# Optimization experiments

Hardware: AMD Instinct MI355X
Metric: run time of the kernel (lower is better)

Reference implementation:

```python
import jax, jax.numpy as jnp
import numpy as np

N_NODES = 100000
N_EDGES = 1600000
N_GRAPHS = 2048
HID = 64
IN_F = 14
N_CLS = 2
EPS = 1e-5


def _gcn_conv(x, row, col, w_edge, W, b, n_nodes):
    # PyG GCNConv with add_self_loops=True, normalize=True.
    xw = x @ W  # [N, out]
    # degree on target nodes, self-loop contributes weight 1
    deg = jnp.zeros((n_nodes,), x.dtype).at[col].add(w_edge) + 1.0
    dinv = deg ** -0.5
    norm = dinv[row] * w_edge * dinv[col]  # [E]
    out = jnp.zeros_like(xw).at[col].add(norm[:, None] * xw[row])
    out = out + (dinv * dinv)[:, None] * xw  # self-loop term
    return out + b


def _bn_relu(x, gamma, beta):
    mean = jnp.mean(x, axis=0)
    var = jnp.var(x, axis=0)  # biased, as PyTorch BN training normalization
    y = gamma * (x - mean) * jax.lax.rsqrt(var + EPS) + beta
    return jax.nn.relu(y)


def setup_inputs() -> dict:
    key = jax.random.key(0)
    ks = jax.random.split(key, 8)
    x = jax.random.normal(ks[0], (N_NODES, IN_F), dtype=jnp.float32)
    edge_index = jax.random.randint(ks[1], (2, N_EDGES), 0, N_NODES, dtype=jnp.int64)
    batch = jnp.sort(jax.random.randint(ks[2], (N_NODES,), 0, N_GRAPHS, dtype=jnp.int64))
    edge_weight = jnp.ones((N_EDGES,), dtype=jnp.float32)
    def lin(k, fi, fo):
        s = 1.0 / np.sqrt(fi)
        kw, kb = jax.random.split(k)
        return (jax.random.uniform(kw, (fi, fo), jnp.float32, -s, s),
                jax.random.uniform(kb, (fo,), jnp.float32, -s, s))
    W1, b1 = lin(ks[3], IN_F, HID)
    W2, b2 = lin(ks[4], HID, HID)
    W3, b3 = lin(ks[5], HID, HID)
    fcW, fcb = lin(ks[6], HID, N_CLS)
    g = jnp.ones((HID,), jnp.float32)
    z = jnp.zeros((HID,), jnp.float32)
    return {
        "x": x, "edge_index": edge_index, "batch": batch, "edge_weight": edge_weight,
        "W1": W1, "b1": b1, "W2": W2, "b2": b2, "W3": W3, "b3": b3,
        "g1": g, "bt1": z, "g2": g, "bt2": z, "g3": g, "bt3": z,
        "fcW": fcW, "fcb": fcb,
    }


def reference(x, edge_index, batch, edge_weight, W1, b1, W2, b2, W3, b3,
              g1, bt1, g2, bt2, g3, bt3, fcW, fcb):
    row, col = edge_index[0], edge_index[1]
    n = x.shape[0]
    h = _bn_relu(_gcn_conv(x, row, col, edge_weight, W1, b1, n), g1, bt1)
    h = _bn_relu(_gcn_conv(h, row, col, edge_weight, W2, b2, n), g2, bt2)
    h = _bn_relu(_gcn_conv(h, row, col, edge_weight, W3, b3, n), g3, bt3)
    node_embs = h  # dropout p=0 is identity
    graph_emb = jax.ops.segment_sum(node_embs, batch, num_segments=N_GRAPHS)
    out = graph_emb @ fcW + fcb
    return (out, node_embs, graph_emb)
```

## Files before the change

kernel.cpp:

```cpp
#include <hip/hip_runtime.h>
#include <hip/hip_fp16.h>

#define N_NODES 100000
#define N_EDGES 1600000
#define EMAX2   1700000
#define N_GRAPHS 2048
#define HID 64
#define IN_F 14
#define N_CLS 2
#define EPS 1e-5f

#define BSHIFT 9
#define NBUCK 196
#define ABLOCKS 256
#define CHUNK (N_EDGES / ABLOCKS)

#define NBLK2 128
#define NCHUNK2 ((N_NODES + NBLK2 - 1) / NBLK2)

typedef _Float16 half_t;
typedef _Float16 half8 __attribute__((ext_vector_type(8)));
typedef float f32x4 __attribute__((ext_vector_type(4)));

#define GSTRIDE ((size_t)N_NODES * 16)


__global__ __launch_bounds__(256) void histA_kernel(const int* __restrict__ col,
                                                    int* __restrict__ histG) {
    __shared__ int hl[NBUCK];
    for (int i = threadIdx.x; i < NBUCK; i += 256) hl[i] = 0;
    __syncthreads();
    int e0 = blockIdx.x * CHUNK;
    for (int e = e0 + threadIdx.x; e < e0 + CHUNK; e += 256)
        atomicAdd(&hl[col[e] >> BSHIFT], 1);
    __syncthreads();
    for (int i = threadIdx.x; i < NBUCK; i += 256)
        histG[i * ABLOCKS + blockIdx.x] = hl[i];
}

__global__ __launch_bounds__(256) void scanS1_kernel(const int* __restrict__ histG,
                                                     int* __restrict__ bsumA) {
    __shared__ int ls[256];
    ls[threadIdx.x] = histG[blockIdx.x * 256 + threadIdx.x];
    __syncthreads();
    for (int off = 128; off > 0; off >>= 1) {
        if (threadIdx.x < off) ls[threadIdx.x] += ls[threadIdx.x + off];
        __syncthreads();
    }
    if (threadIdx.x == 0) bsumA[blockIdx.x] = ls[0];
}

__global__ __launch_bounds__(512) void topscan_kernel(int* __restrict__ bsum, int nb) {
    __shared__ int ls[512];
    int t = threadIdx.x;
    int v = (t < nb) ? bsum[t] : 0;
    ls[t] = v;
    __syncthreads();
    for (int off = 1; off < 512; off <<= 1) {
        int x = ls[t];
        if (t >= off) x += ls[t - off];
        __syncthreads();
        ls[t] = x;
        __syncthreads();
    }
    if (t < nb) bsum[t] = ls[t] - v;
}

__global__ __launch_bounds__(256) void scanS3_kernel(int* __restrict__ histG,
                                                     const int* __restrict__ bsumA,
                                                     int* __restrict__ ptr) {
    __shared__ int ls[256];
    int idx = blockIdx.x * 256 + threadIdx.x;
    int v = histG[idx];
    ls[threadIdx.x] = v;
    __syncthreads();
    for (int off = 1; off < 256; off <<= 1) {
        int x = ls[threadIdx.x];
        if (threadIdx.x >= off) x += ls[threadIdx.x - off];
        __syncthreads();
        ls[threadIdx.x] = x;
        __syncthreads();
    }
    histG[idx] = ls[threadIdx.x] - v + bsumA[blockIdx.x];
    if (blockIdx.x == 0 && threadIdx.x == 0) ptr[N_NODES] = N_EDGES;
}

__global__ __launch_bounds__(256) void scatterA_kernel(const int* __restrict__ row,
                                                       const int* __restrict__ col,
                                                       const float* __restrict__ w,
                                                       const int* __restrict__ histG,
                                                       int2* __restrict__ EA) {
    __shared__ int cur[NBUCK];
    for (int i = threadIdx.x; i < NBUCK; i += 256)
        cur[i] = histG[i * ABLOCKS + blockIdx.x];
    __syncthreads();
    int e0 = blockIdx.x * CHUNK;
    for (int e = e0 + threadIdx.x; e < e0 + CHUNK; e += 256) {
        int c = col[e];
        int r = row[e];
        int fx = (int)__float2uint_rn(w[e] * 8192.0f);
        int pos = atomicAdd(&cur[c >> BSHIFT], 1);
        EA[pos] = make_int2(r, (fx << 17) | c);
    }
}

__global__ __launch_bounds__(256) void bucketA_kernel(const int2* __restrict__ EA,
                                                      const int* __restrict__ bsumA,
                                                      int* __restrict__ ptr,
                                                      float* __restrict__ dinv) {
    __shared__ int hist[512], wsum[512];
    int b = blockIdx.x;
    int beg = bsumA[b];
    int end = (b == NBUCK - 1) ? N_EDGES : bsumA[b + 1];
    int i0 = threadIdx.x, i1 = threadIdx.x + 256;
    hist[i0] = 0; hist[i1] = 0;
    wsum[i0] = 0; wsum[i1] = 0;
    __syncthreads();
    for (int e = beg + threadIdx.x; e < end; e += 256) {
        int2 ed = EA[e];
        int c9 = ed.y & 511;
        atomicAdd(&hist[c9], 1);
        atomicAdd(&wsum[c9], (int)((unsigned int)ed.y >> 17));
    }
    __syncthreads();
    int cnt0 = hist[i0], cnt1 = hist[i1];
    for (int off = 1; off < 512; off <<= 1) {
        int v0 = hist[i0], v1 = hist[i1];
        int a0 = (i0 >= off) ? hist[i0 - off] : 0;
        int a1 = (i1 >= off) ? hist[i1 - off] : 0;
        __syncthreads();
        hist[i0] = v0 + a0;
        hist[i1] = v1 + a1;
        __syncthreads();
    }
    int excl0 = hist[i0] - cnt0, excl1 = hist[i1] - cnt1;
    int col0 = (b << BSHIFT) + i0, col1 = (b << BSHIFT) + i1;
    if (col0 < N_NODES) {
        ptr[col0] = beg + excl0;
        dinv[col0] = rsqrtf(1.0f + (float)wsum[i0] * (1.0f / 8192.0f));
    }
    if (col1 < N_NODES) {
        ptr[col1] = beg + excl1;
        dinv[col1] = rsqrtf(1.0f + (float)wsum[i1] * (1.0f / 8192.0f));
    }
}


__global__ __launch_bounds__(256) void histD_kernel(const int* __restrict__ ptr,
                                                    int* __restrict__ histD) {
    __shared__ int hl[2048];
    for (int i = threadIdx.x; i < 2048; i += 256) hl[i] = 0;
    __syncthreads();
    int n0 = blockIdx.x * NCHUNK2;
    int n1 = n0 + NCHUNK2; if (n1 > N_NODES) n1 = N_NODES;
    for (int n = n0 + threadIdx.x; n < n1; n += 256) {
        int d = ptr[n + 1] - ptr[n];
        if (d > 255) d = 255;
        atomicAdd(&hl[((threadIdx.x & 7) << 8) + d], 1);
    }
    __syncthreads();
    int s = 0;
#pragma unroll
    for (int c = 0; c < 8; c++) s += hl[(c << 8) + threadIdx.x];
    histD[threadIdx.x * NBLK2 + blockIdx.x] = s;
}

__global__ __launch_bounds__(128) void scanD1_kernel(const int* __restrict__ histD,
                                                     int* __restrict__ rowTot) {
    __shared__ int ls[128];
    ls[threadIdx.x] = histD[blockIdx.x * NBLK2 + threadIdx.x];
    __syncthreads();
    for (int off = 64; off > 0; off >>= 1) {
        if (threadIdx.x < off) ls[threadIdx.x] += ls[threadIdx.x + off];
        __syncthreads();
    }
    if (threadIdx.x == 0) rowTot[blockIdx.x] = ls[0];
}

__global__ __launch_bounds__(256) void topscanD_kernel(const int* __restrict__ rowTot,
                                                       int* __restrict__ nodeExcl,
                                                       int* __restrict__ edgeExcl,
                                                       int* __restrict__ ptrS) {
    __shared__ int a[256], b[256];
    int t = threadIdx.x;
    int cnt = rowTot[t];
    int dpad = (t + 1) & ~1;
    int ec = cnt * dpad;
    a[t] = cnt; b[t] = ec;
    __syncthreads();
    for (int off = 1; off < 256; off <<= 1) {
        int va = a[t], vb = b[t];
        if (t >= off) { va += a[t - off]; vb += b[t - off]; }
        __syncthreads();
        a[t] = va; b[t] = vb;
        __syncthreads();
    }
    nodeExcl[t] = a[t] - cnt;
    edgeExcl[t] = b[t] - ec;
    if (t == 255) ptrS[N_NODES] = b[255];
}

__global__ __launch_bounds__(128) void scanD3_kernel(int* __restrict__ histD,
                                                     const int* __restrict__ nodeExcl) {
    __shared__ int ls[128];
    int idx = blockIdx.x * NBLK2 + threadIdx.x;
    int v = histD[idx];
    ls[threadIdx.x] = v;
    __syncthreads();
    for (int off = 1; off < 128; off <<= 1) {
        int x = ls[threadIdx.x];
        if (threadIdx.x >= off) x += ls[threadIdx.x - off];
        __syncthreads();
        ls[threadIdx.x] = x;
        __syncthreads();
    }
    histD[idx] = ls[threadIdx.x] - v + nodeExcl[blockIdx.x];
}

__global__ __launch_bounds__(256) void scatterD_kernel(const int* __restrict__ ptr,
                                                       const int* __restrict__ histD,
                                                       const int* __restrict__ nodeExcl,
                                                       const int* __restrict__ edgeExcl,
                                                       int* __restrict__ perm,
                                                       int* __restrict__ ptrS,
                                                       int* __restrict__ newbase) {
    __shared__ int cur[256];
    cur[threadIdx.x] = histD[threadIdx.x * NBLK2 + blockIdx.x];
    __syncthreads();
    int n0 = blockIdx.x * NCHUNK2;
    int n1 = n0 + NCHUNK2; if (n1 > N_NODES) n1 = N_NODES;
    for (int n = n0 + threadIdx.x; n < n1; n += 256) {
        int d = ptr[n + 1] - ptr[n];
        if (d > 255) d = 255;
        int dpad = (d + 1) & ~1;
        int pos = atomicAdd(&cur[d], 1);
        int ebase = edgeExcl[d] + (pos - nodeExcl[d]) * dpad;
        perm[pos] = n;
        ptrS[pos] = ebase;
        newbase[n] = ebase;
    }
}

__global__ __launch_bounds__(256) void bucketB_kernel(const int2* __restrict__ EA,
                                                      const int* __restrict__ bsumA,
                                                      const int* __restrict__ newbase,
                                                      const float* __restrict__ dinv,
                                                      unsigned int* __restrict__ srcoff,
                                                      half_t* __restrict__ normh) {
    __shared__ int cur[512];
    int b = blockIdx.x;
    int beg = bsumA[b];
    int end = (b == NBUCK - 1) ? N_EDGES : bsumA[b + 1];
    int i0 = threadIdx.x, i1 = threadIdx.x + 256;
    int col0 = (b << BSHIFT) + i0, col1 = (b << BSHIFT) + i1;
    cur[i0] = (col0 < N_NODES) ? newbase[col0] : 0;
    cur[i1] = (col1 < N_NODES) ? newbase[col1] : 0;
    __syncthreads();
    for (int e = beg + threadIdx.x; e < end; e += 256) {
        int2 ed = EA[e];
        int c = ed.y & 0x1ffff;
        float w = (float)((unsigned int)ed.y >> 17) * (1.0f / 8192.0f);
        float nrm = dinv[ed.x] * w * dinv[c];
        int pos = atomicAdd(&cur[c & 511], 1);
        srcoff[pos] = (unsigned int)ed.x << 5;
        normh[pos] = (half_t)nrm;
    }
}


template <int K>
__global__ __launch_bounds__(256) void gemm_kernel(const float* __restrict__ h,
                                                   const float* __restrict__ W,
                                                   half_t* __restrict__ xw, int n_nodes) {
    int f = threadIdx.x & 63;
    float wcol[K];
#pragma unroll
    for (int k = 0; k < K; k++) wcol[k] = W[k * HID + f];
    half_t* xg = xw + (size_t)(f >> 4) * GSTRIDE + (f & 15);
    int wave = (blockIdx.x * blockDim.x + threadIdx.x) >> 6;
    int nwaves = (gridDim.x * blockDim.x) >> 6;
    for (int n = wave; n < n_nodes; n += nwaves) {
        const float* hr = h + (size_t)n * K;
        float acc = 0.f;
#pragma unroll
        for (int k = 0; k < K; k++) acc += hr[k] * wcol[k];
        xg[(size_t)n * 16] = (half_t)acc;
    }
}

__global__ __launch_bounds__(256) void gemm_bn_mfma_kernel(const half_t* __restrict__ h,
                                                           const float* __restrict__ W,
                                                           const float* __restrict__ stats,
                                                           const float* __restrict__ gamma,
                                                           const float* __restrict__ beta,
                                                           half_t* __restrict__ xw, int n_nodes) {
    __shared__ float sc_s[HID], sh_s[HID];
    if (threadIdx.x < 64) {
        float mean = stats[threadIdx.x] * (1.0f / N_NODES);
        float var = stats[64 + threadIdx.x] * (1.0f / N_NODES) - mean * mean;
        float sc = gamma[threadIdx.x] * rsqrtf(var + EPS);
        sc_s[threadIdx.x] = sc;
        sh_s[threadIdx.x] = beta[threadIdx.x] - mean * sc;
    }
    __syncthreads();
    int lane = threadIdx.x & 63;
    int col16 = lane & 15;
    int quad = lane >> 4;

    float scA[2][8], shA[2][8];
#pragma unroll
    for (int kh = 0; kh < 2; kh++)
#pragma unroll
        for (int j = 0; j < 8; j++) {
            int k = kh * 32 + quad * 8 + j;
            scA[kh][j] = sc_s[k];
            shA[kh][j] = sh_s[k];
        }

    half8 bfrag[4][2];
#pragma unroll
    for (int t = 0; t < 4; t++)
#pragma unroll
        for (int kh = 0; kh < 2; kh++)
#pragma unroll
            for (int j = 0; j < 8; j++) {
                int k = kh * 32 + quad * 8 + j;
                bfrag[t][kh][j] = (half_t)W[k * HID + t * 16 + col16];
            }

    int wave = (blockIdx.x * blockDim.x + threadIdx.x) >> 6;
    int nwaves = (gridDim.x * blockDim.x) >> 6;
    int ntiles = n_nodes >> 4;
    for (int tIdx = wave; tIdx < ntiles; tIdx += nwaves) {
        int n0 = tIdx << 4;
        half8 afrag[2];
#pragma unroll
        for (int kh = 0; kh < 2; kh++) {
            int k0 = kh * 32 + quad * 8;
            const half_t* hp = h + (size_t)(k0 >> 4) * GSTRIDE
                                 + (size_t)(n0 + col16) * 16 + (k0 & 15);
            half8 raw = *(const half8*)hp;
#pragma unroll
            for (int j = 0; j < 8; j++) {
                float v = (float)raw[j] * scA[kh][j] + shA[kh][j];
                afrag[kh][j] = (half_t)fmaxf(v, 0.f);
            }
        }
        f32x4 acc[4];
#pragma unroll
        for (int t = 0; t < 4; t++) {
            f32x4 z = {0.f, 0.f, 0.f, 0.f};
            acc[t] = __builtin_amdgcn_mfma_f32_16x16x32_f16(afrag[0], bfrag[t][0], z, 0, 0, 0);
            acc[t] = __builtin_amdgcn_mfma_f32_16x16x32_f16(afrag[1], bfrag[t][1], acc[t], 0, 0, 0);
        }
#pragma unroll
        for (int t = 0; t < 4; t++) {
            half_t* xg = xw + (size_t)t * GSTRIDE;
#pragma unroll
            for (int r = 0; r < 4; r++) {
                int rowi = n0 + quad * 4 + r;
                xg[(size_t)rowi * 16 + col16] = (half_t)acc[t][r];
            }
        }
    }
}

template <bool LAST>
__global__ __launch_bounds__(256) void gather_stats_kernel(const int* __restrict__ ptrS,
                                                           const int* __restrict__ perm,
                                                           const unsigned int* __restrict__ srcoff,
                                                           const unsigned int* __restrict__ normu,
                                                           const half_t* __restrict__ xw,
                                                           const float* __restrict__ dinv,
                                                           const float* __restrict__ b,
                                                           half_t* __restrict__ hp,
                                                           float* __restrict__ hf,
                                                           float* __restrict__ stats,
                                                           int n_nodes) {
    int g = (blockIdx.x & 7) >> 1;
    int grank = ((blockIdx.x >> 3) << 1) | (blockIdx.x & 1);
    int lane16 = threadIdx.x & 15;
    int quadLocal = threadIdx.x >> 4;
    int quadId = grank * 16 + quadLocal;
    int nquads = (gridDim.x >> 2) * 16;

    const half_t* xg = xw + (size_t)g * GSTRIDE;
    const char* xgc = (const char*)xg;
    unsigned int loff = (unsigned int)(lane16 * 2);
    half_t* hpg = hp + (size_t)g * GSTRIDE;
    int f = g * 16 + lane16;
    float bf = b[f];
    int base = ((threadIdx.x & 63) >> 4) * 16;

    float s = 0.f, s2 = 0.f;
    for (int i = quadId; i < n_nodes; i += nquads) {
        int node = perm[i];
        int beg = ptrS[i];
        int c = ptrS[i + 1] - beg;
        __half2 acc0 = __float2half2_rn(0.f);
        __half2 acc1 = __float2half2_rn(0.f);
        for (int j0 = 0; j0 < c; j0 += 16) {
            int m = c - j0;
            if (m > 16) m = 16;
            int pairs = m >> 1;
            int ev = 0, nv = 0;
            if (lane16 < m) ev = (int)srcoff[beg + j0 + lane16];
            if (lane16 < pairs) nv = (int)normu[((beg + j0) >> 1) + lane16];
            int p = 0;
            for (; p + 2 <= pairs; p += 2) {
                unsigned int u0 = (unsigned int)__shfl(ev, base + 2 * p);
                unsigned int u1 = (unsigned int)__shfl(ev, base + 2 * p + 1);
                unsigned int u2 = (unsigned int)__shfl(ev, base + 2 * p + 2);
                unsigned int u3 = (unsigned int)__shfl(ev, base + 2 * p + 3);
                unsigned int nd0 = (unsigned int)__shfl(nv, base + p);
                unsigned int nd1 = (unsigned int)__shfl(nv, base + p + 1);
                __half h0 = *(const __half*)(xgc + (u0 + loff));
                __half h1 = *(const __half*)(xgc + (u1 + loff));
                __half h2 = *(const __half*)(xgc + (u2 + loff));
                __half h3 = *(const __half*)(xgc + (u3 + loff));
                __half2 n01 = *(__half2*)&nd0;
                __half2 n23 = *(__half2*)&nd1;
                acc0 = __hfma2(n01, __halves2half2(h0, h1), acc0);
                acc1 = __hfma2(n23, __halves2half2(h2, h3), acc1);
            }
            if (p < pairs) {
                unsigned int u0 = (unsigned int)__shfl(ev, base + 2 * p);
                unsigned int u1 = (unsigned int)__shfl(ev, base + 2 * p + 1);
                unsigned int nd0 = (unsigned int)__shfl(nv, base + p);
                __half h0 = *(const __half*)(xgc + (u0 + loff));
                __half h1 = *(const __half*)(xgc + (u1 + loff));
                __half2 n01 = *(__half2*)&nd0;
                acc0 = __hfma2(n01, __halves2half2(h0, h1), acc0);
            }
        }
        float accf = (__low2float(acc0) + __high2float(acc0))
                   + (__low2float(acc1) + __high2float(acc1));
        float di = dinv[node];
        float v = accf + di * di * (float)xg[(size_t)node * 16 + lane16] + bf;
        if (LAST)
            hf[(size_t)node * HID + f] = v;
        else
            hpg[(size_t)node * 16 + lane16] = (half_t)v;
        s += v;
        s2 += v * v;
    }
    __shared__ float ls[256], ls2[256];
    ls[threadIdx.x] = s;
    ls2[threadIdx.x] = s2;
    __syncthreads();
    if (threadIdx.x < 16) {
        float a = 0.f, aa = 0.f;
#pragma unroll
        for (int k = 0; k < 16; k++) {
            a += ls[k * 16 + threadIdx.x];
            aa += ls2[k * 16 + threadIdx.x];
        }
        atomicAdd(&stats[g * 16 + threadIdx.x], a);
        atomicAdd(&stats[64 + g * 16 + threadIdx.x], aa);
    }
}

__global__ __launch_bounds__(256) void bn_relu_seg_kernel(float* __restrict__ h,
                                                          const float* __restrict__ stats,
                                                          const float* __restrict__ gamma,
                                                          const float* __restrict__ beta,
                                                          const int* __restrict__ batch,
                                                          float* __restrict__ gemb,
                                                          int n_nodes) {
    int g = blockIdx.x * blockDim.x + threadIdx.x;
    int f = g & 63;
    int wave = g >> 6;
    int nwaves = (gridDim.x * blockDim.x) >> 6;
    int chunk = (n_nodes + nwaves - 1) / nwaves;
    int n0 = wave * chunk;
    int n1 = n0 + chunk;
    if (n1 > n_nodes) n1 = n_nodes;
    if (n0 >= n_nodes) return;
    float mean = stats[f] * (1.0f / N_NODES);
    float var = stats[64 + f] * (1.0f / N_NODES) - mean * mean;
    float sc = gamma[f] * rsqrtf(var + EPS);
    float sh = beta[f] - mean * sc;
    int curg = batch[n0];
    float racc = 0.f;
    for (int n = n0; n < n1; n++) {
        int bg = batch[n];
        if (bg != curg) {
            atomicAdd(&gemb[(size_t)curg * HID + f], racc);
            racc = 0.f;
            curg = bg;
        }
        size_t idx = (size_t)n * HID + f;
        float v = h[idx] * sc + sh;
        v = fmaxf(v, 0.f);
        h[idx] = v;
        racc += v;
    }
    atomicAdd(&gemb[(size_t)curg * HID + f], racc);
}

__global__ __launch_bounds__(256) void final_kernel(const float* __restrict__ gemb,
                                                    const float* __restrict__ fcW,
                                                    const float* __restrict__ fcb,
                                                    float* __restrict__ out) {
    int g = blockIdx.x * blockDim.x + threadIdx.x;
    if (g >= N_GRAPHS * N_CLS) return;
    int gr = g >> 1, c = g & 1;
    float acc = fcb[c];
#pragma unroll
    for (int k = 0; k < HID; k++) acc += gemb[gr * HID + k] * fcW[k * N_CLS + c];
    out[g] = acc;
}


extern "C" void kernel_launch(void* const* d_in, const int* in_sizes, int n_in,
                              void* d_out, int out_size, void* d_ws, size_t ws_size,
                              hipStream_t stream) {
    const float* x    = (const float*)d_in[0];
    const int*   ei   = (const int*)d_in[1];
    const int*   batch= (const int*)d_in[2];
    const float* ew   = (const float*)d_in[3];
    const float* W1   = (const float*)d_in[4];
    const float* b1   = (const float*)d_in[5];
    const float* W2   = (const float*)d_in[6];
    const float* b2   = (const float*)d_in[7];
    const float* W3   = (const float*)d_in[8];
    const float* b3   = (const float*)d_in[9];
    const float* g1   = (const float*)d_in[10];
    const float* bt1  = (const float*)d_in[11];
    const float* g2   = (const float*)d_in[12];
    const float* bt2  = (const float*)d_in[13];
    const float* g3   = (const float*)d_in[14];
    const float* bt3  = (const float*)d_in[15];
    const float* fcW  = (const float*)d_in[16];
    const float* fcb  = (const float*)d_in[17];

    const int* row = ei;
    const int* col = ei + N_EDGES;

    float* out_head  = (float*)d_out;
    float* node_embs = out_head + N_GRAPHS * N_CLS;
    float* gemb      = node_embs + (size_t)N_NODES * HID;

    char* bse = (char*)d_ws;
    half_t* xwh = (half_t*)bse;
    char* r1 = bse + (size_t)N_NODES * HID * 2;
    int2*   EA  = (int2*)r1;
    half_t* hpl = (half_t*)r1;
    char* r2 = r1 + (size_t)N_NODES * HID * 2;
    unsigned int* srcoff = (unsigned int*)r2;
    half_t* normh = (half_t*)(srcoff + EMAX2);
    char* r3 = r2 + (size_t)EMAX2 * 6;
    float* dinv  = (float*)r3;
    float* stats = dinv + N_NODES;
    int*   ptr   = (int*)(stats + 128);
    int*   histG = ptr + N_NODES + 1;
    int*   bsumA = histG + NBUCK * ABLOCKS;
    int*   histD = bsumA + NBUCK + 4;
    int*   rowTot = histD + 256 * NBLK2;
    int*   nodeExcl = rowTot + 256;
    int*   edgeExcl = nodeExcl + 256;
    int*   perm   = edgeExcl + 256;
    int*   newbase= perm + N_NODES;
    int*   ptrS   = newbase + N_NODES;

    const int B   = 256;
    const int gGS = 1024;
    const int gGA = 2048;

    histA_kernel<<<ABLOCKS, B, 0, stream>>>(col, histG);
    scanS1_kernel<<<NBUCK, B, 0, stream>>>(histG, bsumA);
    topscan_kernel<<<1, 512, 0, stream>>>(bsumA, NBUCK);
    scanS3_kernel<<<NBUCK, B, 0, stream>>>(histG, bsumA, ptr);
    scatterA_kernel<<<ABLOCKS, B, 0, stream>>>(row, col, ew, histG, EA);
    bucketA_kernel<<<NBUCK, B, 0, stream>>>(EA, bsumA, ptr, dinv);

    histD_kernel<<<NBLK2, B, 0, stream>>>(ptr, histD);
    scanD1_kernel<<<256, 128, 0, stream>>>(histD, rowTot);
    topscanD_kernel<<<1, 256, 0, stream>>>(rowTot, nodeExcl, edgeExcl, ptrS);
    scanD3_kernel<<<256, 128, 0, stream>>>(histD, nodeExcl);
    scatterD_kernel<<<NBLK2, B, 0, stream>>>(ptr, histD, nodeExcl, edgeExcl,
                                             perm, ptrS, newbase);
    hipMemsetAsync(srcoff, 0, (size_t)EMAX2 * 6, stream);
    bucketB_kernel<<<NBUCK, B, 0, stream>>>(EA, bsumA, newbase, dinv, srcoff, normh);

    float* h3 = node_embs;

    gemm_kernel<IN_F><<<gGS, B, 0, stream>>>(x, W1, xwh, N_NODES);
    hipMemsetAsync(stats, 0, 128 * sizeof(float), stream);
    gather_stats_kernel<false><<<gGA, B, 0, stream>>>(ptrS, perm, srcoff,
                                                      (const unsigned int*)normh, xwh,
                                                      dinv, b1, hpl, h3, stats, N_NODES);

    gemm_bn_mfma_kernel<<<gGS, B, 0, stream>>>(hpl, W2, stats, g1, bt1, xwh, N_NODES);
    hipMemsetAsync(stats, 0, 128 * sizeof(float), stream);
    gather_stats_kernel<false><<<gGA, B, 0, stream>>>(ptrS, perm, srcoff,
                                                      (const unsigned int*)normh, xwh,
                                                      dinv, b2, hpl, h3, stats, N_NODES);

    gemm_bn_mfma_kernel<<<gGS, B, 0, stream>>>(hpl, W3, stats, g2, bt2, xwh, N_NODES);
    hipMemsetAsync(stats, 0, 128 * sizeof(float), stream);
    gather_stats_kernel<true><<<gGA, B, 0, stream>>>(ptrS, perm, srcoff,
                                                     (const unsigned int*)normh, xwh,
                                                     dinv, b3, hpl, h3, stats, N_NODES);

    hipMemsetAsync(gemb, 0, (size_t)N_GRAPHS * HID * sizeof(float), stream);
    bn_relu_seg_kernel<<<gGS, B, 0, stream>>>(h3, stats, g3, bt3, batch, gemb, N_NODES);

    final_kernel<<<(N_GRAPHS * N_CLS + B - 1) / B, B, 0, stream>>>(gemb, fcW, fcb, out_head);
}
```

Before: 415.0 us.

## Pad per-node edge lists to multiples of four and use vector loads in gather

Edge slots per node are now padded to a multiple of four instead of two. This lets the gather loop read source offsets and norms with 128-bit and 64-bit per-lane vector loads instead of cooperative loads plus shuffles, and the loop is unrolled over 16 edges with four accumulators. The per-layer stats memsets are merged into a single upfront memset of three separate stats buffers, and the gemb memset is moved up with them. The cost is more padded zero edges (larger buffer, wasted loads) and redundant per-lane index loads across the 16 lanes.

```diff
diff --git a/kernel.cpp b/kernel.cpp
--- a/kernel.cpp
+++ b/kernel.cpp
@@ -3,7 +3,7 @@
 
 #define N_NODES 100000
 #define N_EDGES 1600000
-#define EMAX2   1700000
+#define EMAX4   1900000
 #define N_GRAPHS 2048
 #define HID 64
 #define IN_F 14
@@ -21,8 +21,17 @@
 typedef _Float16 half_t;
 typedef _Float16 half8 __attribute__((ext_vector_type(8)));
 typedef float f32x4 __attribute__((ext_vector_type(4)));
+typedef unsigned int u32;
+typedef u32 u32x4 __attribute__((ext_vector_type(4)));
+typedef u32 u32x2 __attribute__((ext_vector_type(2)));
 
 #define GSTRIDE ((size_t)N_NODES * 16)
+
+__device__ __forceinline__ __half2 u32_as_half2(u32 u) {
+    union { u32 u; __half2 h; } c;
+    c.u = u;
+    return c.h;
+}
 
 
 __global__ __launch_bounds__(256) void histA_kernel(const int* __restrict__ col,
@@ -184,7 +193,7 @@
     __shared__ int a[256], b[256];
     int t = threadIdx.x;
     int cnt = rowTot[t];
-    int dpad = (t + 1) & ~1;
+    int dpad = (t + 3) & ~3;
     int ec = cnt * dpad;
     a[t] = cnt; b[t] = ec;
     __syncthreads();
@@ -232,7 +241,7 @@
     for (int n = n0 + threadIdx.x; n < n1; n += 256) {
         int d = ptr[n + 1] - ptr[n];
         if (d > 255) d = 255;
-        int dpad = (d + 1) & ~1;
+        int dpad = (d + 3) & ~3;
         int pos = atomicAdd(&cur[d], 1);
         int ebase = edgeExcl[d] + (pos - nodeExcl[d]) * dpad;
         perm[pos] = n;
@@ -369,7 +378,7 @@
 __global__ __launch_bounds__(256) void gather_stats_kernel(const int* __restrict__ ptrS,
                                                            const int* __restrict__ perm,
                                                            const unsigned int* __restrict__ srcoff,
-                                                           const unsigned int* __restrict__ normu,
+                                                           const half_t* __restrict__ normh,
                                                            const half_t* __restrict__ xw,
                                                            const float* __restrict__ dinv,
                                                            const float* __restrict__ b,
@@ -387,54 +396,65 @@
     const half_t* xg = xw + (size_t)g * GSTRIDE;
     const char* xgc = (const char*)xg;
     unsigned int loff = (unsigned int)(lane16 * 2);
+    const unsigned int* np = (const unsigned int*)normh;
     half_t* hpg = hp + (size_t)g * GSTRIDE;
     int f = g * 16 + lane16;
     float bf = b[f];
-    int base = ((threadIdx.x & 63) >> 4) * 16;
 
     float s = 0.f, s2 = 0.f;
     for (int i = quadId; i < n_nodes; i += nquads) {
         int node = perm[i];
-        int beg = ptrS[i];
-        int c = ptrS[i + 1] - beg;
-        __half2 acc0 = __float2half2_rn(0.f);
-        __half2 acc1 = __float2half2_rn(0.f);
-        for (int j0 = 0; j0 < c; j0 += 16) {
-            int m = c - j0;
-            if (m > 16) m = 16;
-            int pairs = m >> 1;
-            int ev = 0, nv = 0;
-            if (lane16 < m) ev = (int)srcoff[beg + j0 + lane16];
-            if (lane16 < pairs) nv = (int)normu[((beg + j0) >> 1) + lane16];
-            int p = 0;
-            for (; p + 2 <= pairs; p += 2) {
-                unsigned int u0 = (unsigned int)__shfl(ev, base + 2 * p);
-                unsigned int u1 = (unsigned int)__shfl(ev, base + 2 * p + 1);
-                unsigned int u2 = (unsigned int)__shfl(ev, base + 2 * p + 2);
-                unsigned int u3 = (unsigned int)__shfl(ev, base + 2 * p + 3);
-                unsigned int nd0 = (unsigned int)__shfl(nv, base + p);
-                unsigned int nd1 = (unsigned int)__shfl(nv, base + p + 1);
-                __half h0 = *(const __half*)(xgc + (u0 + loff));
-                __half h1 = *(const __half*)(xgc + (u1 + loff));
-                __half h2 = *(const __half*)(xgc + (u2 + loff));
-                __half h3 = *(const __half*)(xgc + (u3 + loff));
-                __half2 n01 = *(__half2*)&nd0;
-                __half2 n23 = *(__half2*)&nd1;
-                acc0 = __hfma2(n01, __halves2half2(h0, h1), acc0);
-                acc1 = __hfma2(n23, __halves2half2(h2, h3), acc1);
-            }
-            if (p < pairs) {
-                unsigned int u0 = (unsigned int)__shfl(ev, base + 2 * p);
-                unsigned int u1 = (unsigned int)__shfl(ev, base + 2 * p + 1);
-                unsigned int nd0 = (unsigned int)__shfl(nv, base + p);
-                __half h0 = *(const __half*)(xgc + (u0 + loff));
-                __half h1 = *(const __half*)(xgc + (u1 + loff));
-                __half2 n01 = *(__half2*)&nd0;
-                acc0 = __hfma2(n01, __halves2half2(h0, h1), acc0);
-            }
-        }
-        float accf = (__low2float(acc0) + __high2float(acc0))
-                   + (__low2float(acc1) + __high2float(acc1));
+        int j = ptrS[i];
+        int cend = ptrS[i + 1];
+        __half2 z2 = __float2half2_rn(0.f);
+        __half2 acc0 = z2, acc1 = z2, acc2 = z2, acc3 = z2;
+        for (; j + 16 <= cend; j += 16) {
+            u32x4 s0 = *(const u32x4*)(srcoff + j);
+            u32x4 s1 = *(const u32x4*)(srcoff + j + 4);
+            u32x4 s2v = *(const u32x4*)(srcoff + j + 8);
+            u32x4 s3 = *(const u32x4*)(srcoff + j + 12);
+            int jh = j >> 1;
+            u32x2 n0 = *(const u32x2*)(np + jh);
+            u32x2 n1 = *(const u32x2*)(np + jh + 2);
+            u32x2 n2 = *(const u32x2*)(np + jh + 4);
+            u32x2 n3 = *(const u32x2*)(np + jh + 6);
+            __half h0 = *(const __half*)(xgc + (s0.x + loff));
+            __half h1 = *(const __half*)(xgc + (s0.y + loff));
+            __half h2 = *(const __half*)(xgc + (s0.z + loff));
+            __half h3 = *(const __half*)(xgc + (s0.w + loff));
+            __half h4 = *(const __half*)(xgc + (s1.x + loff));
+            __half h5 = *(const __half*)(xgc + (s1.y + loff));
+            __half h6 = *(const __half*)(xgc + (s1.z + loff));
+            __half h7 = *(const __half*)(xgc + (s1.w + loff));
+            __half h8 = *(const __half*)(xgc + (s2v.x + loff));
+            __half h9 = *(const __half*)(xgc + (s2v.y + loff));
+            __half hA = *(const __half*)(xgc + (s2v.z + loff));
+            __half hB = *(const __half*)(xgc + (s2v.w + loff));
+            __half hC = *(const __half*)(xgc + (s3.x + loff));
+            __half hD = *(const __half*)(xgc + (s3.y + loff));
+            __half hE = *(const __half*)(xgc + (s3.z + loff));
+            __half hF = *(const __half*)(xgc + (s3.w + loff));
+            acc0 = __hfma2(u32_as_half2(n0.x), __halves2half2(h0, h1), acc0);
+            acc0 = __hfma2(u32_as_half2(n0.y), __halves2half2(h2, h3), acc0);
+            acc1 = __hfma2(u32_as_half2(n1.x), __halves2half2(h4, h5), acc1);
+            acc1 = __hfma2(u32_as_half2(n1.y), __halves2half2(h6, h7), acc1);
+            acc2 = __hfma2(u32_as_half2(n2.x), __halves2half2(h8, h9), acc2);
+            acc2 = __hfma2(u32_as_half2(n2.y), __halves2half2(hA, hB), acc2);
+            acc3 = __hfma2(u32_as_half2(n3.x), __halves2half2(hC, hD), acc3);
+            acc3 = __hfma2(u32_as_half2(n3.y), __halves2half2(hE, hF), acc3);
+        }
+        for (; j < cend; j += 4) {
+            u32x4 s0 = *(const u32x4*)(srcoff + j);
+            u32x2 n0 = *(const u32x2*)(np + (j >> 1));
+            __half h0 = *(const __half*)(xgc + (s0.x + loff));
+            __half h1 = *(const __half*)(xgc + (s0.y + loff));
+            __half h2 = *(const __half*)(xgc + (s0.z + loff));
+            __half h3 = *(const __half*)(xgc + (s0.w + loff));
+            acc0 = __hfma2(u32_as_half2(n0.x), __halves2half2(h0, h1), acc0);
+            acc1 = __hfma2(u32_as_half2(n0.y), __halves2half2(h2, h3), acc1);
+        }
+        __half2 accp = __hadd2(__hadd2(acc0, acc1), __hadd2(acc2, acc3));
+        float accf = __low2float(accp) + __high2float(accp);
         float di = dinv[node];
         float v = accf + di * di * (float)xg[(size_t)node * 16 + lane16] + bf;
         if (LAST)
@@ -548,11 +568,11 @@
     half_t* hpl = (half_t*)r1;
     char* r2 = r1 + (size_t)N_NODES * HID * 2;
     unsigned int* srcoff = (unsigned int*)r2;
-    half_t* normh = (half_t*)(srcoff + EMAX2);
-    char* r3 = r2 + (size_t)EMAX2 * 6;
+    half_t* normh = (half_t*)(srcoff + EMAX4);
+    char* r3 = r2 + (size_t)EMAX4 * 6;
     float* dinv  = (float*)r3;
-    float* stats = dinv + N_NODES;
-    int*   ptr   = (int*)(stats + 128);
+    float* stats3 = dinv + N_NODES;
+    int*   ptr   = (int*)(stats3 + 384);
     int*   histG = ptr + N_NODES + 1;
     int*   bsumA = histG + NBUCK * ABLOCKS;
     int*   histD = bsumA + NBUCK + 4;
@@ -580,31 +600,26 @@
     scanD3_kernel<<<256, 128, 0, stream>>>(histD, nodeExcl);
     scatterD_kernel<<<NBLK2, B, 0, stream>>>(ptr, histD, nodeExcl, edgeExcl,
                                              perm, ptrS, newbase);
-    hipMemsetAsync(srcoff, 0, (size_t)EMAX2 * 6, stream);
+    hipMemsetAsync(srcoff, 0, (size_t)EMAX4 * 6, stream);
+    hipMemsetAsync(stats3, 0, 384 * sizeof(float), stream);
+    hipMemsetAsync(gemb, 0, (size_t)N_GRAPHS * HID * sizeof(float), stream);
     bucketB_kernel<<<NBUCK, B, 0, stream>>>(EA, bsumA, newbase, dinv, srcoff, normh);
 
     float* h3 = node_embs;
 
     gemm_kernel<IN_F><<<gGS, B, 0, stream>>>(x, W1, xwh, N_NODES);
-    hipMemsetAsync(stats, 0, 128 * sizeof(float), stream);
-    gather_stats_kernel<false><<<gGA, B, 0, stream>>>(ptrS, perm, srcoff,
-                                                      (const unsigned int*)normh, xwh,
-                                                      dinv, b1, hpl, h3, stats, N_NODES);
-
-    gemm_bn_mfma_kernel<<<gGS, B, 0, stream>>>(hpl, W2, stats, g1, bt1, xwh, N_NODES);
-    hipMemsetAsync(stats, 0, 128 * sizeof(float), stream);
-    gather_stats_kernel<false><<<gGA, B, 0, stream>>>(ptrS, perm, srcoff,
-                                                      (const unsigned int*)normh, xwh,
-                                                      dinv, b2, hpl, h3, stats, N_NODES);
-
-    gemm_bn_mfma_kernel<<<gGS, B, 0, stream>>>(hpl, W3, stats, g2, bt2, xwh, N_NODES);
-    hipMemsetAsync(stats, 0, 128 * sizeof(float), stream);
-    gather_stats_kernel<true><<<gGA, B, 0, stream>>>(ptrS, perm, srcoff,
-                                                     (const unsigned int*)normh, xwh,
-                                                     dinv, b3, hpl, h3, stats, N_NODES);
-
-    hipMemsetAsync(gemb, 0, (size_t)N_GRAPHS * HID * sizeof(float), stream);
-    bn_relu_seg_kernel<<<gGS, B, 0, stream>>>(h3, stats, g3, bt3, batch, gemb, N_NODES);
+    gather_stats_kernel<false><<<gGA, B, 0, stream>>>(ptrS, perm, srcoff, normh, xwh,
+                                                      dinv, b1, hpl, h3, stats3, N_NODES);
+
+    gemm_bn_mfma_kernel<<<gGS, B, 0, stream>>>(hpl, W2, stats3, g1, bt1, xwh, N_NODES);
+    gather_stats_kernel<false><<<gGA, B, 0, stream>>>(ptrS, perm, srcoff, normh, xwh,
+                                                      dinv, b2, hpl, h3, stats3 + 128, N_NODES);
+
+    gemm_bn_mfma_kernel<<<gGS, B, 0, stream>>>(hpl, W3, stats3 + 128, g2, bt2, xwh, N_NODES);
+    gather_stats_kernel<true><<<gGA, B, 0, stream>>>(ptrS, perm, srcoff, normh, xwh,
+                                                     dinv, b3, hpl, h3, stats3 + 256, N_NODES);
+
+    bn_relu_seg_kernel<<<gGS, B, 0, stream>>>(h3, stats3 + 256, g3, bt3, batch, gemb, N_NODES);
 
     final_kernel<<<(N_GRAPHS * N_CLS + B - 1) / B, B, 0, stream>>>(gemb, fcW, fcb, out_head);
 }
```

Measured after the change: 432.8 us. 4.3% more time.
